# Kernel optimization log

Hardware: AMD Instinct MI355X
Metric: run time of the kernel (lower is better)

## Reference

```python
import jax, jax.numpy as jnp
import numpy as np

B, N, IN_DIM, HD, K, L = 8, 3072, 3, 64, 16, 2


def setup_inputs() -> dict:
    key = jax.random.key(0)
    ks = jax.random.split(key, 16)
    s = lambda k, shp, fan: jax.random.normal(k, shp, jnp.float32) / np.sqrt(fan)
    return {
        "x": jax.random.normal(ks[0], (B, N, IN_DIM), jnp.float32),
        "datanorm": jnp.ones((IN_DIM,), jnp.float32),
        "W_in": s(ks[1], (IN_DIM, HD), IN_DIM), "b_in": jnp.zeros((HD,), jnp.float32),
        "W1": s(ks[2], (L, 2 * HD, 2 * HD), 2 * HD), "b1": jnp.zeros((L, 2 * HD), jnp.float32),
        "W2": s(ks[3], (L, 2 * HD, HD), 2 * HD), "b2": jnp.zeros((L, HD), jnp.float32),
        "Wo1": s(ks[4], (HD, HD), HD), "bo1": jnp.zeros((HD,), jnp.float32),
        "Wo2": s(ks[5], (HD, HD), HD), "bo2": jnp.zeros((HD,), jnp.float32),
        "Wo3": s(ks[6], (HD, 1), HD), "bo3": jnp.zeros((1,), jnp.float32),
    }


def _knn_idx(h, k):
    # h: [B, N, D]; squared euclidean dists per graph; loop=True so self (d=0) is kept
    xx = jnp.sum(h * h, axis=-1)                      # [B, N]
    d2 = xx[:, :, None] + xx[:, None, :] - 2.0 * jnp.einsum("bnd,bmd->bnm", h, h)
    _, idx = jax.lax.top_k(-d2, k)                    # [B, N, K] nearest (incl. self)
    return idx


def reference(x, datanorm, W_in, b_in, W1, b1, W2, b2, Wo1, bo1, Wo2, bo2, Wo3, bo3):
    # input net: datanorm scale + Linear + ELU
    h = jax.nn.elu((x * datanorm) @ W_in + b_in)      # [B, N, HD]
    for l in range(L):
        idx = _knn_idx(h, K)                          # dynamic kNN graph on current features
        xj = jax.vmap(lambda hb, ib: hb[ib])(h, idx)  # [B, N, K, HD] gather neighbors
        xi = h[:, :, None, :]
        msg = jnp.concatenate([jnp.broadcast_to(xi, xj.shape), xj - xi], axis=-1)  # [B,N,K,2HD]
        m = jax.nn.elu(msg @ W1[l] + b1[l])
        m = jax.nn.elu(m @ W2[l] + b2[l])             # [B, N, K, HD]
        h = jnp.sum(m, axis=2)                        # EdgeConv aggr='add'
    pooled = jnp.max(h, axis=1)                       # global_max_pool per graph -> [B, HD]
    o = jax.nn.elu(pooled @ Wo1 + bo1)
    o = jax.nn.elu(o @ Wo2 + bo2)
    return o @ Wo3 + bo3                              # [B, 1]
```

## Files before the change

kernel.cpp:

```cpp
#include <hip/hip_runtime.h>
#include <cstdint>

#define NB 8
#define NN 3072
#define HD 64
#define KK 16
#define NL 2
#define ROWS_TOT (NB * NN)

typedef unsigned long long u64;
typedef __attribute__((ext_vector_type(8))) short short8;
typedef __attribute__((ext_vector_type(4))) float f32x4;

__device__ __forceinline__ float elu_f(float x) {
  return x > 0.0f ? x : __expf(x) - 1.0f;
}

__device__ __forceinline__ unsigned sortkey(float f) {
  unsigned u = __float_as_uint(f);
  unsigned m = ((unsigned)((int)u >> 31)) | 0x80000000u;
  return u ^ m;
}

__device__ __forceinline__ void split_bf16(float f, unsigned& hb, unsigned& lb) {
  unsigned u = __float_as_uint(f);
  hb = (u + 0x7fffu + ((u >> 16) & 1u)) >> 16;
  float hif = __uint_as_float(hb << 16);
  float lo = f - hif;
  unsigned ul = __float_as_uint(lo);
  lb = (ul + 0x7fffu + ((ul >> 16) & 1u)) >> 16;
}

__device__ __forceinline__ unsigned short bf16rne(float f) {
  unsigned u = __float_as_uint(f);
  return (unsigned short)((u + 0x7fffu + ((u >> 16) & 1u)) >> 16);
}

__device__ __forceinline__ void gl_lds16(const void* g, void* l) {
  __builtin_amdgcn_global_load_lds(
      (const __attribute__((address_space(1))) unsigned int*)g,
      (__attribute__((address_space(3))) unsigned int*)l, 16, 0, 0);
}

__global__ void k_embed(const float* __restrict__ x, const float* __restrict__ dn,
                        const float* __restrict__ Win, const float* __restrict__ bin,
                        float* __restrict__ h) {
  const int t = threadIdx.x;
  const int row = blockIdx.x * 4 + (t >> 6);
  const int d = t & 63;
  const float* xr = x + (size_t)row * 3;
  float a = bin[d];
#pragma unroll
  for (int c = 0; c < 3; ++c) a = fmaf(xr[c] * dn[c], Win[c * HD + d], a);
  h[(size_t)row * HD + d] = elu_f(a);
}

__global__ void k_split(const float* __restrict__ h, unsigned short* __restrict__ hhi,
                        unsigned short* __restrict__ hlo, float* __restrict__ xx) {
  __shared__ float xsum[32];
  const int t = threadIdx.x;
  const int C = blockIdx.x * 256 + t;
  const int Rg = C >> 10;
  const int within = C & 1023;
  const int rt16 = within >> 7;
  const int kc = (within >> 6) & 1;
  const int quad = (within >> 4) & 3;
  const int row = within & 15;
  const int lr = ((t >> 7) & 1) * 16 + (t & 15);
  const int r = Rg * 128 + rt16 * 16 + row;
  const int k0 = kc * 32 + quad * 8;
  const float* src = h + (size_t)r * HD + k0;
  if (t < 32) xsum[t] = 0.0f;
  __syncthreads();
  unsigned hh[8], ll[8];
  float ss = 0.0f;
#pragma unroll
  for (int j = 0; j < 8; ++j) {
    const float f = src[j];
    ss = fmaf(f, f, ss);
    split_bf16(f, hh[j], ll[j]);
  }
  atomicAdd(&xsum[lr], ss);
  uint4 oh, ol;
  oh.x = hh[0] | (hh[1] << 16); oh.y = hh[2] | (hh[3] << 16);
  oh.z = hh[4] | (hh[5] << 16); oh.w = hh[6] | (hh[7] << 16);
  ol.x = ll[0] | (ll[1] << 16); ol.y = ll[2] | (ll[3] << 16);
  ol.z = ll[4] | (ll[5] << 16); ol.w = ll[6] | (ll[7] << 16);
  *(uint4*)(hhi + (size_t)C * 8) = oh;
  *(uint4*)(hlo + (size_t)C * 8) = ol;
  __syncthreads();
  if (((t >> 4) & 7) == 0) xx[r] = xsum[lr];
}

__global__ void k_packw(const float* __restrict__ W1, const float* __restrict__ W2,
                        unsigned short* __restrict__ w0h, unsigned short* __restrict__ w0l,
                        unsigned short* __restrict__ w1h, unsigned short* __restrict__ w2h) {
  const int cid = blockIdx.x * 256 + threadIdx.x;
  const int l = cid / 3072;
  const int r = cid % 3072;
  const int lane = r & 63;
  if (r < 1024) {
    const int c = r;
    const int nt = c >> 7, kc = (c >> 6) & 1;
    const int k0 = kc * 32 + (lane >> 4) * 8;
    const int n = nt * 16 + (lane & 15);
    unsigned hh[8], ll[8];
#pragma unroll
    for (int j = 0; j < 8; ++j) split_bf16(W1[(size_t)l * 16384 + (k0 + j) * 128 + n], hh[j], ll[j]);
    unsigned short* dh = w0h + ((size_t)l * 1024 + c) * 8;
    unsigned short* dl = w0l + ((size_t)l * 1024 + c) * 8;
#pragma unroll
    for (int j = 0; j < 8; ++j) { dh[j] = (unsigned short)hh[j]; dl[j] = (unsigned short)ll[j]; }
  } else if (r < 2048) {
    const int c = r - 1024;
    const int nt = c >> 7, kc = (c >> 6) & 1;
    const int k0 = 64 + kc * 32 + (lane >> 4) * 8;
    const int n = nt * 16 + (lane & 15);
    unsigned short* dh = w1h + ((size_t)l * 1024 + c) * 8;
#pragma unroll
    for (int j = 0; j < 8; ++j) dh[j] = bf16rne(W1[(size_t)l * 16384 + (k0 + j) * 128 + n]);
  } else {
    const int c = r - 2048;
    const int nt = c >> 8, kc = (c >> 6) & 3;
    const int k0 = kc * 32 + (lane >> 4) * 8;
    const int n = nt * 16 + (lane & 15);
    unsigned short* dh = w2h + ((size_t)l * 1024 + c) * 8;
#pragma unroll
    for (int j = 0; j < 8; ++j) dh[j] = bf16rne(W2[(size_t)l * 8192 + (k0 + j) * 64 + n]);
  }
}

__global__ __launch_bounds__(256) void k_stat(const unsigned short* __restrict__ hhi,
                                              const unsigned short* __restrict__ hlo,
                                              const float* __restrict__ xx,
                                              float* __restrict__ tilemin) {
  __shared__ __align__(16) unsigned short Bh[2][4096], Bl[2][4096];
  __shared__ float smin[128 * 13];
  const int t = threadIdx.x;
  const int bg = blockIdx.x / 96;
  const int rem = blockIdx.x % 96;
  const int qg = rem / 4, cq = rem % 4;
  const int w = t >> 6, lane = t & 63;
  const int lane16 = lane & 15, quad = lane >> 4;
  const float* xxb = xx + (size_t)bg * NN;

  short8 afh[2][2], afl[2][2];
  {
    const size_t base = ((size_t)bg * 24 + qg) * 8192;
#pragma unroll
    for (int mt = 0; mt < 2; ++mt)
#pragma unroll
      for (int kc = 0; kc < 2; ++kc) {
        const size_t off = base + (size_t)(w * 2 + mt) * 1024 + kc * 512 + lane * 8;
        afh[mt][kc] = *(const short8*)(hhi + off);
        afl[mt][kc] = *(const short8*)(hlo + off);
      }
  }
#define STAGE(cb, bsel)                                                       \
  {                                                                           \
    const size_t bb = ((size_t)bg * 24 + ((cb) >> 1)) * 8192 +                \
                      (size_t)((cb) & 1) * 4096;                              \
    const char* sH = (const char*)(hhi + bb);                                 \
    const char* sL = (const char*)(hlo + bb);                                 \
    char* dH = (char*)&Bh[bsel][0];                                           \
    char* dL = (char*)&Bl[bsel][0];                                           \
    const int o1 = t * 16, o2 = t * 16 + 4096;                                \
    gl_lds16(sH + o1, dH + o1);                                               \
    gl_lds16(sH + o2, dH + o2);                                               \
    gl_lds16(sL + o1, dL + o1);                                               \
    gl_lds16(sL + o2, dL + o2);                                               \
  }

  STAGE(cq * 12, 0);
  __syncthreads();
  for (int it = 0; it < 12; ++it) {
    const int cb = cq * 12 + it;
    if (it + 1 < 12) STAGE(cb + 1, (it + 1) & 1);
    const unsigned short* bhp = Bh[it & 1];
    const unsigned short* blp = Bl[it & 1];
    f32x4 acc[2][4];
#pragma unroll
    for (int mt = 0; mt < 2; ++mt)
#pragma unroll
      for (int nt = 0; nt < 4; ++nt) acc[mt][nt] = (f32x4){0.f, 0.f, 0.f, 0.f};
#pragma unroll
    for (int kc = 0; kc < 2; ++kc)
#pragma unroll
      for (int nt = 0; nt < 4; ++nt) {
        const int off = nt * 1024 + kc * 512 + lane * 8;
        const short8 bh = *(const short8*)&bhp[off];
        const short8 bl = *(const short8*)&blp[off];
#pragma unroll
        for (int mt = 0; mt < 2; ++mt) {
          acc[mt][nt] = __builtin_amdgcn_mfma_f32_16x16x32_bf16(afh[mt][kc], bh, acc[mt][nt], 0, 0, 0);
          acc[mt][nt] = __builtin_amdgcn_mfma_f32_16x16x32_bf16(afh[mt][kc], bl, acc[mt][nt], 0, 0, 0);
          acc[mt][nt] = __builtin_amdgcn_mfma_f32_16x16x32_bf16(afl[mt][kc], bh, acc[mt][nt], 0, 0, 0);
        }
      }
    float rm[2][4];
#pragma unroll
    for (int mt = 0; mt < 2; ++mt)
#pragma unroll
      for (int r = 0; r < 4; ++r) rm[mt][r] = 3.402823466e+38f;
#pragma unroll
    for (int nt = 0; nt < 4; ++nt) {
      const float xc = xxb[cb * 64 + nt * 16 + lane16];
#pragma unroll
      for (int mt = 0; mt < 2; ++mt)
#pragma unroll
        for (int r = 0; r < 4; ++r)
          rm[mt][r] = fminf(rm[mt][r], fmaf(-2.0f, acc[mt][nt][r], xc));
    }
#pragma unroll
    for (int mask = 1; mask <= 8; mask <<= 1)
#pragma unroll
      for (int mt = 0; mt < 2; ++mt)
#pragma unroll
        for (int r = 0; r < 4; ++r)
          rm[mt][r] = fminf(rm[mt][r], __shfl_xor(rm[mt][r], mask, 64));
#pragma unroll
    for (int mt = 0; mt < 2; ++mt) {
      float v = rm[mt][0];
      v = (lane16 == 1) ? rm[mt][1] : v;
      v = (lane16 == 2) ? rm[mt][2] : v;
      v = (lane16 == 3) ? rm[mt][3] : v;
      if (lane16 < 4) {
        const int row = w * 32 + mt * 16 + quad * 4 + lane16;
        smin[row * 13 + it] = v;
      }
    }
    __syncthreads();
  }
  if (t < 128) {
    float* dst = tilemin + ((size_t)bg * NN + qg * 128 + t) * 48 + cq * 12;
    const float* src = &smin[t * 13];
    *(float4*)dst = (float4){src[0], src[1], src[2], src[3]};
    *(float4*)(dst + 4) = (float4){src[4], src[5], src[6], src[7]};
    *(float4*)(dst + 8) = (float4){src[8], src[9], src[10], src[11]};
  }
}

__global__ __launch_bounds__(256) void k_thresh(const float* __restrict__ tilemin,
                                                float* __restrict__ T,
                                                int* __restrict__ cnt) {
  __shared__ float sb[4][64];
  const int t = threadIdx.x, w = t >> 6, lane = t & 63;
  const int row = blockIdx.x * 4 + w;
  const float v = (lane < 48) ? tilemin[(size_t)row * 48 + lane] : 3.402823466e+38f;
  sb[w][lane] = v;
  int rank = 0;
  for (int i = 0; i < 48; ++i) {
    const float s = sb[w][i];
    rank += (s < v) || (s == v && i < lane);
  }
  if (lane < 48 && rank == 15) T[row] = v;
  if (lane == 0) cnt[row] = 0;
}

__global__ __launch_bounds__(256) void k_compact(const unsigned short* __restrict__ hhi,
                                                 const unsigned short* __restrict__ hlo,
                                                 const float* __restrict__ xx,
                                                 const float* __restrict__ T,
                                                 int* __restrict__ cnt,
                                                 u64* __restrict__ surv) {
  __shared__ __align__(16) unsigned short Bh[2][4096], Bl[2][4096];
  __shared__ u64 lsurv[128 * 20];
  __shared__ int lcnt[128];
  const int t = threadIdx.x;
  const int bg = blockIdx.x / 96;
  const int rem = blockIdx.x % 96;
  const int qg = rem / 4, cq = rem % 4;
  const int w = t >> 6, lane = t & 63;
  const int lane16 = lane & 15, quad = lane >> 4;
  const float* xxb = xx + (size_t)bg * NN;
  const int rowbase = bg * NN + qg * 128 + w * 32;

  short8 afh[2][2], afl[2][2];
  {
    const size_t base = ((size_t)bg * 24 + qg) * 8192;
#pragma unroll
    for (int mt = 0; mt < 2; ++mt)
#pragma unroll
      for (int kc = 0; kc < 2; ++kc) {
        const size_t off = base + (size_t)(w * 2 + mt) * 1024 + kc * 512 + lane * 8;
        afh[mt][kc] = *(const short8*)(hhi + off);
        afl[mt][kc] = *(const short8*)(hlo + off);
      }
  }
  float Tr[2][4];
#pragma unroll
  for (int mt = 0; mt < 2; ++mt)
#pragma unroll
    for (int r = 0; r < 4; ++r) Tr[mt][r] = T[rowbase + mt * 16 + quad * 4 + r];
  if (t < 128) lcnt[t] = 0;

  STAGE(cq * 12, 0);
  __syncthreads();
  for (int it = 0; it < 12; ++it) {
    const int cb = cq * 12 + it;
    if (it + 1 < 12) STAGE(cb + 1, (it + 1) & 1);
    const unsigned short* bhp = Bh[it & 1];
    const unsigned short* blp = Bl[it & 1];
    f32x4 acc[2][4];
#pragma unroll
    for (int mt = 0; mt < 2; ++mt)
#pragma unroll
      for (int nt = 0; nt < 4; ++nt) acc[mt][nt] = (f32x4){0.f, 0.f, 0.f, 0.f};
#pragma unroll
    for (int kc = 0; kc < 2; ++kc)
#pragma unroll
      for (int nt = 0; nt < 4; ++nt) {
        const int off = nt * 1024 + kc * 512 + lane * 8;
        const short8 bh = *(const short8*)&bhp[off];
        const short8 bl = *(const short8*)&blp[off];
#pragma unroll
        for (int mt = 0; mt < 2; ++mt) {
          acc[mt][nt] = __builtin_amdgcn_mfma_f32_16x16x32_bf16(afh[mt][kc], bh, acc[mt][nt], 0, 0, 0);
          acc[mt][nt] = __builtin_amdgcn_mfma_f32_16x16x32_bf16(afh[mt][kc], bl, acc[mt][nt], 0, 0, 0);
          acc[mt][nt] = __builtin_amdgcn_mfma_f32_16x16x32_bf16(afl[mt][kc], bh, acc[mt][nt], 0, 0, 0);
        }
      }
#pragma unroll
    for (int nt = 0; nt < 4; ++nt) {
      const float xc = xxb[cb * 64 + nt * 16 + lane16];
#pragma unroll
      for (int mt = 0; mt < 2; ++mt)
#pragma unroll
        for (int r = 0; r < 4; ++r) {
          const float d = fmaf(-2.0f, acc[mt][nt][r], xc);
          if (d <= Tr[mt][r]) {
            const int rloc = w * 32 + mt * 16 + quad * 4 + r;
            const int idx = atomicAdd(&lcnt[rloc], 1);
            if (idx < 20)
              lsurv[rloc * 20 + idx] =
                  ((u64)sortkey(d) << 32) | (unsigned)(cb * 64 + nt * 16 + lane16);
          }
        }
    }
    __syncthreads();
  }
#undef STAGE
  if (t < 128) {
    const int row = bg * NN + qg * 128 + t;
    int myc = lcnt[t];
    myc = myc > 20 ? 20 : myc;
    const int base = atomicAdd(&cnt[row], myc);
    for (int i = 0; i < myc; ++i) {
      const int pos = base + i;
      if (pos < 96) surv[(size_t)row * 96 + pos] = lsurv[t * 20 + i];
    }
  }
}

__global__ __launch_bounds__(256) void k_rank(const u64* __restrict__ surv,
                                              const int* __restrict__ cnt,
                                              int* __restrict__ knn) {
  __shared__ u64 sb[4][96];
  const int t = threadIdx.x, w = t >> 6, lane = t & 63;
  const int row = blockIdx.x * 4 + w;
  int c = cnt[row];
  c = c > 96 ? 96 : c;
  const u64 m0 = (lane < c) ? surv[(size_t)row * 96 + lane] : ~0ull;
  const u64 m1 = (64 + lane < c) ? surv[(size_t)row * 96 + 64 + lane] : ~0ull;
  sb[w][lane] = m0;
  if (lane < 32) sb[w][64 + lane] = m1;
  int r0 = 0, r1 = 0;
  for (int i = 0; i < c; ++i) {
    const u64 sv = sb[w][i];
    r0 += (sv < m0) ? 1 : 0;
    r1 += (sv < m1) ? 1 : 0;
  }
  if (lane < c && r0 < KK)
    knn[(size_t)row * KK + r0] = (int)(unsigned)(m0 & 0xffffffffu);
  if (lane < 32 && 64 + lane < c && r1 < KK)
    knn[(size_t)row * KK + r1] = (int)(unsigned)(m1 & 0xffffffffu);
}

__global__ __launch_bounds__(256, 2) void k_base(const unsigned short* __restrict__ hhi,
                                                 const unsigned short* __restrict__ hlo,
                                                 const unsigned short* __restrict__ w0h,
                                                 const unsigned short* __restrict__ w0l,
                                                 const float* __restrict__ b1l,
                                                 float* __restrict__ base1) {
  __shared__ unsigned short Ah[8192], Al[8192];
  const int t = threadIdx.x;
  const int grp = blockIdx.x;
  {
    const uint4* sah = (const uint4*)(hhi + (size_t)grp * 8192);
    const uint4* sal = (const uint4*)(hlo + (size_t)grp * 8192);
#pragma unroll
    for (int i = 0; i < 4; ++i) {
      ((uint4*)Ah)[t + 256 * i] = sah[t + 256 * i];
      ((uint4*)Al)[t + 256 * i] = sal[t + 256 * i];
    }
  }
  __syncthreads();
  const int w = t >> 6, lane = t & 63;
  const int lane16 = lane & 15, quad = lane >> 4;
  f32x4 acc[2][8];
#pragma unroll
  for (int mt = 0; mt < 2; ++mt)
#pragma unroll
    for (int nt = 0; nt < 8; ++nt) {
      const float bv = b1l[nt * 16 + lane16];
      acc[mt][nt] = (f32x4){bv, bv, bv, bv};
    }
#pragma unroll
  for (int kc = 0; kc < 2; ++kc)
#pragma unroll
    for (int mt = 0; mt < 2; ++mt) {
      const int offA = (((w * 2 + mt) * 2 + kc) * 64 + lane) * 8;
      const short8 ah = *(const short8*)&Ah[offA];
      const short8 al = *(const short8*)&Al[offA];
#pragma unroll
      for (int nt = 0; nt < 8; ++nt) {
        const int offB = ((nt * 2 + kc) * 64 + lane) * 8;
        const short8 bh = *(const short8*)(w0h + offB);
        const short8 bl = *(const short8*)(w0l + offB);
        acc[mt][nt] = __builtin_amdgcn_mfma_f32_16x16x32_bf16(ah, bh, acc[mt][nt], 0, 0, 0);
        acc[mt][nt] = __builtin_amdgcn_mfma_f32_16x16x32_bf16(ah, bl, acc[mt][nt], 0, 0, 0);
        acc[mt][nt] = __builtin_amdgcn_mfma_f32_16x16x32_bf16(al, bh, acc[mt][nt], 0, 0, 0);
      }
    }
#pragma unroll
  for (int mt = 0; mt < 2; ++mt)
#pragma unroll
    for (int nt = 0; nt < 8; ++nt) {
      const int row = (w * 2 + mt) * 16 + quad * 4;
      const int col = nt * 16 + lane16;
#pragma unroll
      for (int r = 0; r < 4; ++r)
        base1[((size_t)grp * 128 + row + r) * 128 + col] = acc[mt][nt][r];
    }
}

__global__ __launch_bounds__(256, 4) void k_msg3(
    const float* __restrict__ h, const int* __restrict__ knn,
    const float* __restrict__ base1, const float* __restrict__ b2l,
    const unsigned short* __restrict__ w1h, const unsigned short* __restrict__ w2h,
    float* __restrict__ hout) {
  __shared__ unsigned short A1[4096];
  __shared__ unsigned short m1b[8192];
  __shared__ float hloc[256];
  __shared__ float base1L[512];
  const int t = threadIdx.x;
  const int b = blockIdx.x / (NN / 4);
  const int p0 = (blockIdx.x % (NN / 4)) * 4;
  const float* hb = h + (size_t)b * NN * HD;

  if (t < 64) {
    const int p = t >> 4, c4 = t & 15;
    *(float4*)&hloc[p * 64 + c4 * 4] = *(const float4*)(hb + (size_t)(p0 + p) * HD + c4 * 4);
  }
  if (t < 128)
    *(float4*)&base1L[t * 4] = *(const float4*)(base1 + ((size_t)b * NN + p0) * 128 + t * 4);
  __syncthreads();

  {
    const int e = t >> 2, qs = t & 3;
    const int p = e >> 4, m = e & 15;
    const int j = knn[((size_t)b * NN + p0 + p) * KK + m];
    const float* hj = hb + (size_t)j * HD + qs * 16;
    const int kc = qs >> 1;
#pragma unroll
    for (int half = 0; half < 2; ++half) {
      const int c0 = qs * 16 + half * 8;
      const int quad = (c0 >> 3) & 3;
      const float4 va = *(const float4*)(hj + half * 8);
      const float4 vb = *(const float4*)(hj + half * 8 + 4);
      const float4 ia = *(const float4*)&hloc[p * 64 + c0];
      const float4 ib = *(const float4*)&hloc[p * 64 + c0 + 4];
      const float d[8] = {va.x - ia.x, va.y - ia.y, va.z - ia.z, va.w - ia.w,
                          vb.x - ib.x, vb.y - ib.y, vb.z - ib.z, vb.w - ib.w};
      unsigned r8[8];
#pragma unroll
      for (int jj = 0; jj < 8; ++jj) r8[jj] = bf16rne(d[jj]);
      uint4 o;
      o.x = r8[0] | (r8[1] << 16); o.y = r8[2] | (r8[3] << 16);
      o.z = r8[4] | (r8[5] << 16); o.w = r8[6] | (r8[7] << 16);
      *(uint4*)&A1[((p * 2 + kc) * 64 + quad * 16 + m) * 8] = o;
    }
  }
  __syncthreads();

  const int w = t >> 6, lane = t & 63;
  const int lane16 = lane & 15, quad = lane >> 4;

  f32x4 acc1[8];
#pragma unroll
  for (int nt = 0; nt < 8; ++nt) {
    const float bv = base1L[w * 128 + nt * 16 + lane16];
    acc1[nt] = (f32x4){bv, bv, bv, bv};
  }
  short8 a1[2];
#pragma unroll
  for (int kc = 0; kc < 2; ++kc) a1[kc] = *(const short8*)&A1[((w * 2 + kc) * 64 + lane) * 8];
#pragma unroll
  for (int kc = 0; kc < 2; ++kc)
#pragma unroll
    for (int nt = 0; nt < 8; ++nt) {
      const short8 bh = *(const short8*)(w1h + ((nt * 2 + kc) * 64 + lane) * 8);
      acc1[nt] = __builtin_amdgcn_mfma_f32_16x16x32_bf16(a1[kc], bh, acc1[nt], 0, 0, 0);
    }
#pragma unroll
  for (int nt = 0; nt < 8; ++nt) {
    const int c = nt * 16 + lane16;
    const int boff = w * 2048 + (c >> 5) * 512 + ((c >> 3) & 3) * 128 + (c & 7);
#pragma unroll
    for (int r = 0; r < 4; ++r)
      m1b[boff + (quad * 4 + r) * 8] = bf16rne(elu_f(acc1[nt][r]));
  }
  __syncthreads();

  f32x4 acc2[4];
#pragma unroll
  for (int nt = 0; nt < 4; ++nt) {
    const float bv = b2l[nt * 16 + lane16];
    acc2[nt] = (f32x4){bv, bv, bv, bv};
  }
#pragma unroll
  for (int kc = 0; kc < 4; ++kc) {
    const short8 a2 = *(const short8*)&m1b[w * 2048 + kc * 512 + quad * 128 + lane16 * 8];
#pragma unroll
    for (int nt = 0; nt < 4; ++nt) {
      const short8 bh = *(const short8*)(w2h + ((nt * 4 + kc) * 64 + lane) * 8);
      acc2[nt] = __builtin_amdgcn_mfma_f32_16x16x32_bf16(a2, bh, acc2[nt], 0, 0, 0);
    }
  }
#pragma unroll
  for (int nt = 0; nt < 4; ++nt) {
    float s = elu_f(acc2[nt][0]) + elu_f(acc2[nt][1]) + elu_f(acc2[nt][2]) + elu_f(acc2[nt][3]);
    s += __shfl_xor(s, 16, 64);
    s += __shfl_xor(s, 32, 64);
    if (quad == 0) hout[((size_t)b * NN + p0 + w) * HD + nt * 16 + lane16] = s;
  }
}

__global__ void k_pool(const float* __restrict__ h, float* __restrict__ part) {
  __shared__ float red[4][64];
  const int t = threadIdx.x;
  const int gidx = blockIdx.x;
  const int b = gidx / 24, seg = gidx % 24;
  const int q = t >> 6, d = t & 63;
  const float* hb = h + ((size_t)b * NN + seg * 128) * HD;
  float m = -3.402823466e+38f;
  for (int n = q; n < 128; n += 4) m = fmaxf(m, hb[(size_t)n * HD + d]);
  red[q][d] = m;
  __syncthreads();
  if (t < 64)
    part[(size_t)gidx * HD + t] =
        fmaxf(fmaxf(red[0][t], red[1][t]), fmaxf(red[2][t], red[3][t]));
}

__global__ void k_head2(const float* __restrict__ part, const float* __restrict__ Wo1,
                        const float* __restrict__ bo1, const float* __restrict__ Wo2,
                        const float* __restrict__ bo2, const float* __restrict__ Wo3,
                        const float* __restrict__ bo3, float* __restrict__ out) {
  __shared__ float pooled[64];
  __shared__ float o1[64];
  __shared__ float o2s[64];
  const int t = threadIdx.x;
  const int b = blockIdx.x;
  if (t < 64) {
    float m = -3.402823466e+38f;
    for (int g = 0; g < 24; ++g) m = fmaxf(m, part[((size_t)b * 24 + g) * HD + t]);
    pooled[t] = m;
  }
  __syncthreads();
  if (t < 64) {
    float a = bo1[t];
    for (int c = 0; c < 64; ++c) a = fmaf(pooled[c], Wo1[c * 64 + t], a);
    o1[t] = elu_f(a);
  }
  __syncthreads();
  if (t < 64) {
    float a = bo2[t];
    for (int c = 0; c < 64; ++c) a = fmaf(o1[c], Wo2[c * 64 + t], a);
    o2s[t] = elu_f(a);
  }
  __syncthreads();
  if (t < 64) {
    float v = o2s[t] * Wo3[t];
#pragma unroll
    for (int mm = 32; mm >= 1; mm >>= 1) v += __shfl_xor(v, mm, 64);
    if (t == 0) out[b] = v + bo3[0];
  }
}

extern "C" void kernel_launch(void* const* d_in, const int* in_sizes, int n_in,
                              void* d_out, int out_size, void* d_ws, size_t ws_size,
                              hipStream_t stream) {
  const float* x   = (const float*)d_in[0];
  const float* dn  = (const float*)d_in[1];
  const float* Win = (const float*)d_in[2];
  const float* bin = (const float*)d_in[3];
  const float* W1  = (const float*)d_in[4];
  const float* b1  = (const float*)d_in[5];
  const float* W2  = (const float*)d_in[6];
  const float* b2  = (const float*)d_in[7];
  const float* Wo1 = (const float*)d_in[8];
  const float* bo1 = (const float*)d_in[9];
  const float* Wo2 = (const float*)d_in[10];
  const float* bo2 = (const float*)d_in[11];
  const float* Wo3 = (const float*)d_in[12];
  const float* bo3 = (const float*)d_in[13];
  float* out = (float*)d_out;

  char* p = (char*)d_ws;
  const size_t hbytes = (size_t)NB * NN * HD * 4;
  float* h0 = (float*)p; p += hbytes;
  float* h1 = (float*)p; p += hbytes;
  float* xx = (float*)p; p += (size_t)NB * NN * 4;
  int* knn  = (int*)p;   p += (size_t)NB * NN * KK * 4;
  unsigned short* hhi = (unsigned short*)p; p += (size_t)NB * NN * HD * 2;
  unsigned short* hlo = (unsigned short*)p; p += (size_t)NB * NN * HD * 2;
  unsigned short* w0h = (unsigned short*)p; p += (size_t)NL * 8192 * 2;
  unsigned short* w0l = (unsigned short*)p; p += (size_t)NL * 8192 * 2;
  unsigned short* w1h = (unsigned short*)p; p += (size_t)NL * 8192 * 2;
  unsigned short* w2h = (unsigned short*)p; p += (size_t)NL * 8192 * 2;
  float* part = (float*)p; p += (size_t)NB * 24 * HD * 4;
  float* tilemin = (float*)p; p += (size_t)48 * ROWS_TOT * 4;
  float* Tthr = (float*)p; p += (size_t)ROWS_TOT * 4;
  int* scnt = (int*)p; p += (size_t)ROWS_TOT * 4;
  u64* surv = (u64*)p; p += (size_t)ROWS_TOT * 96 * 8;
  float* base1 = (float*)p; p += (size_t)NB * NN * 128 * 4;

  const int rows = NB * NN;
  k_embed<<<rows / 4, 256, 0, stream>>>(x, dn, Win, bin, h0);
  k_packw<<<NL * 3072 / 256, 256, 0, stream>>>(W1, W2, w0h, w0l, w1h, w2h);
  float* hin = h0;
  float* hbuf = h1;
  for (int l = 0; l < NL; ++l) {
    k_split<<<rows * HD / 8 / 256, 256, 0, stream>>>(hin, hhi, hlo, xx);
    k_stat<<<NB * 96, 256, 0, stream>>>(hhi, hlo, xx, tilemin);
    k_thresh<<<rows / 4, 256, 0, stream>>>(tilemin, Tthr, scnt);
    k_compact<<<NB * 96, 256, 0, stream>>>(hhi, hlo, xx, Tthr, scnt, surv);
    k_rank<<<rows / 4, 256, 0, stream>>>(surv, scnt, knn);
    k_base<<<rows / 128, 256, 0, stream>>>(hhi, hlo, w0h + (size_t)l * 8192,
                                           w0l + (size_t)l * 8192, b1 + l * 128, base1);
    k_msg3<<<rows / 4, 256, 0, stream>>>(hin, knn, base1, b2 + l * 64,
                                         w1h + (size_t)l * 8192, w2h + (size_t)l * 8192,
                                         hbuf);
    float* tmp = hin; hin = hbuf; hbuf = tmp;
  }
  k_pool<<<NB * 24, 256, 0, stream>>>(hin, part);
  k_head2<<<NB, 256, 0, stream>>>(part, Wo1, bo1, Wo2, bo2, Wo3, bo3, out);
}
```

Measured before the change: 393.5 us.

## Fuse embed with bf16 split and rank selection into message kernel

The input embedding kernel now also writes the hi/lo bf16 split and squared norms directly, so the first layer's split kernel is skipped. The k_rank kernel is removed and its rank-by-count selection of the 16 nearest survivors runs inside k_msg3, one wave per point, with results kept in shared memory instead of a global knn buffer. This removes three kernel launches and a global round trip of the neighbor indices. In exchange k_msg3 uses more shared memory and does extra work before its first barrier, which could lower occupancy.

```diff
diff --git a/kernel.cpp b/kernel.cpp
--- a/kernel.cpp
+++ b/kernel.cpp
@@ -42,17 +42,54 @@
       (__attribute__((address_space(3))) unsigned int*)l, 16, 0, 0);
 }
 
-__global__ void k_embed(const float* __restrict__ x, const float* __restrict__ dn,
-                        const float* __restrict__ Win, const float* __restrict__ bin,
-                        float* __restrict__ h) {
-  const int t = threadIdx.x;
-  const int row = blockIdx.x * 4 + (t >> 6);
-  const int d = t & 63;
-  const float* xr = x + (size_t)row * 3;
-  float a = bin[d];
-#pragma unroll
-  for (int c = 0; c < 3; ++c) a = fmaf(xr[c] * dn[c], Win[c * HD + d], a);
-  h[(size_t)row * HD + d] = elu_f(a);
+__global__ void k_embed2(const float* __restrict__ x, const float* __restrict__ dn,
+                         const float* __restrict__ Win, const float* __restrict__ bin,
+                         float* __restrict__ h, unsigned short* __restrict__ hhi,
+                         unsigned short* __restrict__ hlo, float* __restrict__ xx) {
+  __shared__ float xsum[32];
+  const int t = threadIdx.x;
+  const int C = blockIdx.x * 256 + t;
+  const int Rg = C >> 10;
+  const int within = C & 1023;
+  const int rt16 = within >> 7;
+  const int kc = (within >> 6) & 1;
+  const int quad = (within >> 4) & 3;
+  const int row = within & 15;
+  const int lr = ((t >> 7) & 1) * 16 + (t & 15);
+  const int r = Rg * 128 + rt16 * 16 + row;
+  const int k0 = kc * 32 + quad * 8;
+  if (t < 32) xsum[t] = 0.0f;
+  __syncthreads();
+  const float xd0 = x[(size_t)r * 3 + 0] * dn[0];
+  const float xd1 = x[(size_t)r * 3 + 1] * dn[1];
+  const float xd2 = x[(size_t)r * 3 + 2] * dn[2];
+  unsigned hh[8], ll[8];
+  float hv[8];
+  float ss = 0.0f;
+#pragma unroll
+  for (int j = 0; j < 8; ++j) {
+    const int d = k0 + j;
+    float a = bin[d];
+    a = fmaf(xd0, Win[d], a);
+    a = fmaf(xd1, Win[HD + d], a);
+    a = fmaf(xd2, Win[2 * HD + d], a);
+    const float f = elu_f(a);
+    hv[j] = f;
+    ss = fmaf(f, f, ss);
+    split_bf16(f, hh[j], ll[j]);
+  }
+  atomicAdd(&xsum[lr], ss);
+  *(float4*)(h + (size_t)r * HD + k0) = (float4){hv[0], hv[1], hv[2], hv[3]};
+  *(float4*)(h + (size_t)r * HD + k0 + 4) = (float4){hv[4], hv[5], hv[6], hv[7]};
+  uint4 oh, ol;
+  oh.x = hh[0] | (hh[1] << 16); oh.y = hh[2] | (hh[3] << 16);
+  oh.z = hh[4] | (hh[5] << 16); oh.w = hh[6] | (hh[7] << 16);
+  ol.x = ll[0] | (ll[1] << 16); ol.y = ll[2] | (ll[3] << 16);
+  ol.z = ll[4] | (ll[5] << 16); ol.w = ll[6] | (ll[7] << 16);
+  *(uint4*)(hhi + (size_t)C * 8) = oh;
+  *(uint4*)(hlo + (size_t)C * 8) = ol;
+  __syncthreads();
+  if (((t >> 4) & 7) == 0) xx[r] = xsum[lr];
 }
 
 __global__ void k_split(const float* __restrict__ h, unsigned short* __restrict__ hhi,
@@ -352,30 +389,6 @@
   }
 }
 
-__global__ __launch_bounds__(256) void k_rank(const u64* __restrict__ surv,
-                                              const int* __restrict__ cnt,
-                                              int* __restrict__ knn) {
-  __shared__ u64 sb[4][96];
-  const int t = threadIdx.x, w = t >> 6, lane = t & 63;
-  const int row = blockIdx.x * 4 + w;
-  int c = cnt[row];
-  c = c > 96 ? 96 : c;
-  const u64 m0 = (lane < c) ? surv[(size_t)row * 96 + lane] : ~0ull;
-  const u64 m1 = (64 + lane < c) ? surv[(size_t)row * 96 + 64 + lane] : ~0ull;
-  sb[w][lane] = m0;
-  if (lane < 32) sb[w][64 + lane] = m1;
-  int r0 = 0, r1 = 0;
-  for (int i = 0; i < c; ++i) {
-    const u64 sv = sb[w][i];
-    r0 += (sv < m0) ? 1 : 0;
-    r1 += (sv < m1) ? 1 : 0;
-  }
-  if (lane < c && r0 < KK)
-    knn[(size_t)row * KK + r0] = (int)(unsigned)(m0 & 0xffffffffu);
-  if (lane < 32 && 64 + lane < c && r1 < KK)
-    knn[(size_t)row * KK + r1] = (int)(unsigned)(m1 & 0xffffffffu);
-}
-
 __global__ __launch_bounds__(256, 2) void k_base(const unsigned short* __restrict__ hhi,
                                                  const unsigned short* __restrict__ hlo,
                                                  const unsigned short* __restrict__ w0h,
@@ -435,7 +448,8 @@
 }
 
 __global__ __launch_bounds__(256, 4) void k_msg3(
-    const float* __restrict__ h, const int* __restrict__ knn,
+    const float* __restrict__ h, const int* __restrict__ cnt,
+    const u64* __restrict__ surv,
     const float* __restrict__ base1, const float* __restrict__ b2l,
     const unsigned short* __restrict__ w1h, const unsigned short* __restrict__ w2h,
     float* __restrict__ hout) {
@@ -443,10 +457,14 @@
   __shared__ unsigned short m1b[8192];
   __shared__ float hloc[256];
   __shared__ float base1L[512];
+  __shared__ u64 sbr[4][96];
+  __shared__ int knnL[4][16];
   const int t = threadIdx.x;
   const int b = blockIdx.x / (NN / 4);
   const int p0 = (blockIdx.x % (NN / 4)) * 4;
   const float* hb = h + (size_t)b * NN * HD;
+  const int w = t >> 6, lane = t & 63;
+  const int lane16 = lane & 15, quad = lane >> 4;
 
   if (t < 64) {
     const int p = t >> 4, c4 = t & 15;
@@ -454,18 +472,38 @@
   }
   if (t < 128)
     *(float4*)&base1L[t * 4] = *(const float4*)(base1 + ((size_t)b * NN + p0) * 128 + t * 4);
+
+  {
+    const int row = b * NN + p0 + w;
+    if (lane < 16) knnL[w][lane] = 0;
+    int c = cnt[row];
+    c = c > 96 ? 96 : c;
+    const u64 m0 = (lane < c) ? surv[(size_t)row * 96 + lane] : ~0ull;
+    const u64 m1 = (64 + lane < c) ? surv[(size_t)row * 96 + 64 + lane] : ~0ull;
+    sbr[w][lane] = m0;
+    if (lane < 32) sbr[w][64 + lane] = m1;
+    int r0 = 0, r1 = 0;
+    for (int i = 0; i < c; ++i) {
+      const u64 sv = sbr[w][i];
+      r0 += (sv < m0) ? 1 : 0;
+      r1 += (sv < m1) ? 1 : 0;
+    }
+    if (lane < c && r0 < KK) knnL[w][r0] = (int)(unsigned)(m0 & 0xffffffffu);
+    if (lane < 32 && 64 + lane < c && r1 < KK)
+      knnL[w][r1] = (int)(unsigned)(m1 & 0xffffffffu);
+  }
   __syncthreads();
 
   {
     const int e = t >> 2, qs = t & 3;
     const int p = e >> 4, m = e & 15;
-    const int j = knn[((size_t)b * NN + p0 + p) * KK + m];
+    const int j = knnL[p][m];
     const float* hj = hb + (size_t)j * HD + qs * 16;
     const int kc = qs >> 1;
 #pragma unroll
     for (int half = 0; half < 2; ++half) {
       const int c0 = qs * 16 + half * 8;
-      const int quad = (c0 >> 3) & 3;
+      const int qd = (c0 >> 3) & 3;
       const float4 va = *(const float4*)(hj + half * 8);
       const float4 vb = *(const float4*)(hj + half * 8 + 4);
       const float4 ia = *(const float4*)&hloc[p * 64 + c0];
@@ -478,13 +516,10 @@
       uint4 o;
       o.x = r8[0] | (r8[1] << 16); o.y = r8[2] | (r8[3] << 16);
       o.z = r8[4] | (r8[5] << 16); o.w = r8[6] | (r8[7] << 16);
-      *(uint4*)&A1[((p * 2 + kc) * 64 + quad * 16 + m) * 8] = o;
-    }
-  }
-  __syncthreads();
-
-  const int w = t >> 6, lane = t & 63;
-  const int lane16 = lane & 15, quad = lane >> 4;
+      *(uint4*)&A1[((p * 2 + kc) * 64 + qd * 16 + m) * 8] = o;
+    }
+  }
+  __syncthreads();
 
   f32x4 acc1[8];
 #pragma unroll
@@ -611,7 +646,6 @@
   float* h0 = (float*)p; p += hbytes;
   float* h1 = (float*)p; p += hbytes;
   float* xx = (float*)p; p += (size_t)NB * NN * 4;
-  int* knn  = (int*)p;   p += (size_t)NB * NN * KK * 4;
   unsigned short* hhi = (unsigned short*)p; p += (size_t)NB * NN * HD * 2;
   unsigned short* hlo = (unsigned short*)p; p += (size_t)NB * NN * HD * 2;
   unsigned short* w0h = (unsigned short*)p; p += (size_t)NL * 8192 * 2;
@@ -626,19 +660,19 @@
   float* base1 = (float*)p; p += (size_t)NB * NN * 128 * 4;
 
   const int rows = NB * NN;
-  k_embed<<<rows / 4, 256, 0, stream>>>(x, dn, Win, bin, h0);
   k_packw<<<NL * 3072 / 256, 256, 0, stream>>>(W1, W2, w0h, w0l, w1h, w2h);
+  k_embed2<<<rows * HD / 8 / 256, 256, 0, stream>>>(x, dn, Win, bin, h0, hhi, hlo, xx);
   float* hin = h0;
   float* hbuf = h1;
   for (int l = 0; l < NL; ++l) {
-    k_split<<<rows * HD / 8 / 256, 256, 0, stream>>>(hin, hhi, hlo, xx);
+    if (l > 0)
+      k_split<<<rows * HD / 8 / 256, 256, 0, stream>>>(hin, hhi, hlo, xx);
     k_stat<<<NB * 96, 256, 0, stream>>>(hhi, hlo, xx, tilemin);
     k_thresh<<<rows / 4, 256, 0, stream>>>(tilemin, Tthr, scnt);
     k_compact<<<NB * 96, 256, 0, stream>>>(hhi, hlo, xx, Tthr, scnt, surv);
-    k_rank<<<rows / 4, 256, 0, stream>>>(surv, scnt, knn);
     k_base<<<rows / 128, 256, 0, stream>>>(hhi, hlo, w0h + (size_t)l * 8192,
                                            w0l + (size_t)l * 8192, b1 + l * 128, base1);
-    k_msg3<<<rows / 4, 256, 0, stream>>>(hin, knn, base1, b2 + l * 64,
+    k_msg3<<<rows / 4, 256, 0, stream>>>(hin, scnt, surv, base1, b2 + l * 64,
                                          w1h + (size_t)l * 8192, w2h + (size_t)l * 8192,
                                          hbuf);
     float* tmp = hin; hin = hbuf; hbuf = tmp;
```

Result: faster. 384.4 us (-2.3%).
